# Optimization experiments

Measured on AMD Instinct MI355X. Metric: run time of the kernel, lower is better.

Reference implementation:

```python
import jax, jax.numpy as jnp
import numpy as np

NUM_HEADS = 16
EPS = 1e-6  # LinearAttention.epsilon

def setup_inputs() -> dict:
    key = jax.random.key(0)
    ks = jax.random.split(key, 10)
    B, L, D = 4, 4096, 2048
    s = 1.0 / np.sqrt(D)
    x = jax.random.normal(ks[0], (B, L, D), dtype=jnp.float32)
    attention_mask = jnp.ones((B, L), dtype=jnp.float32)
    Wq = jax.random.normal(ks[1], (D, D), dtype=jnp.float32) * s
    bq = jnp.zeros((D,), dtype=jnp.float32)
    Wk = jax.random.normal(ks[2], (D, D), dtype=jnp.float32) * s
    bk = jnp.zeros((D,), dtype=jnp.float32)
    Wv = jax.random.normal(ks[3], (D, D), dtype=jnp.float32) * s
    bv = jnp.zeros((D,), dtype=jnp.float32)
    Wo = jax.random.normal(ks[4], (D, D), dtype=jnp.float32) * s
    bo = jnp.zeros((D,), dtype=jnp.float32)
    return {"x": x, "attention_mask": attention_mask, "Wq": Wq, "bq": bq,
            "Wk": Wk, "bk": bk, "Wv": Wv, "bv": bv, "Wo": Wo, "bo": bo}

def reference(x, attention_mask, Wq, bq, Wk, bk, Wv, bv, Wo, bo):
    B, L, Dm = x.shape
    H = NUM_HEADS
    Dh = Dm // H
    # q/k/v projections -> [B, H, L, Dh]
    def proj(W, b):
        return (x @ W + b).reshape(B, L, H, Dh).transpose(0, 2, 1, 3)
    q = proj(Wq, bq)
    k = proj(Wk, bk)
    v = proj(Wv, bv)
    # feature map: elu(x) + 1
    q = jax.nn.elu(q) + 1.0
    k = jax.nn.elu(k) + 1.0
    # mask keys/values: mask [B, 1, L, 1]
    m = attention_mask[:, None, :, None]
    k = k * m
    v = v * m
    # causal linear attention via cumulative sums over sequence dim
    k_cum = jnp.cumsum(k, axis=2)          # [B,H,L,Dh]
    kv_cum = jnp.cumsum(k * v, axis=2)     # [B,H,L,Dh] (diagonal kv state, as in source)
    z = jnp.sum(q * k_cum, axis=-1) + EPS  # [B,H,L]
    z = z * attention_mask[:, None, :]
    out = (q * kv_cum) / z[..., None]      # [B,H,L,Dh]
    out = out.transpose(0, 2, 1, 3).reshape(B, L, Dm)
    return out @ Wo + bo
```

## Files before the change

kernel.cpp:

```cpp
#include <hip/hip_runtime.h>
#include <cstdint>
#include <cstddef>

#define EPS_F 1e-6f

__device__ inline unsigned short f2bf(float f) {
    union { float f; unsigned u; } v; v.f = f;
    unsigned r = v.u + 0x7fffu + ((v.u >> 16) & 1u);
    return (unsigned short)(r >> 16);
}
__device__ inline float bf2f(unsigned u16) {
    union { unsigned u; float f; } v; v.u = u16 << 16; return v.f;
}

typedef __attribute__((ext_vector_type(8))) __bf16 bf16x8;
typedef __attribute__((ext_vector_type(8))) short short8;
typedef __attribute__((ext_vector_type(4))) float floatx4;

__device__ inline void async_load16(const void* g, void* l) {
    __builtin_amdgcn_global_load_lds((const __attribute__((address_space(1))) void*)g,
                                     (__attribute__((address_space(3))) void*)l,
                                     16, 0, 0);
}

__global__ void cast_x_kernel(const float* __restrict__ in, unsigned short* __restrict__ out, int n8) {
    int i = blockIdx.x * blockDim.x + threadIdx.x;
    if (i < n8) {
        float4 a = ((const float4*)in)[2 * i];
        float4 b = ((const float4*)in)[2 * i + 1];
        short8 o;
        o[0] = (short)f2bf(a.x); o[1] = (short)f2bf(a.y);
        o[2] = (short)f2bf(a.z); o[3] = (short)f2bf(a.w);
        o[4] = (short)f2bf(b.x); o[5] = (short)f2bf(b.y);
        o[6] = (short)f2bf(b.z); o[7] = (short)f2bf(b.w);
        ((short8*)out)[i] = o;
    }
}

__global__ void transpose_cast_kernel(const float* __restrict__ W0, const float* __restrict__ W1,
                                      const float* __restrict__ W2, const float* __restrict__ W3,
                                      unsigned short* __restrict__ WtBase, int n) {
    const float* W = (blockIdx.z == 0) ? W0 : (blockIdx.z == 1) ? W1 : (blockIdx.z == 2) ? W2 : W3;
    unsigned short* Wt = WtBase + (size_t)blockIdx.z * n * n;
    __shared__ float tile[32][33];
    int bx = blockIdx.x * 32;
    int by = blockIdx.y * 32;
    int tx = threadIdx.x;
    int ty = threadIdx.y;
    #pragma unroll
    for (int i = 0; i < 32; i += 8)
        tile[ty + i][tx] = W[(size_t)(by + ty + i) * n + bx + tx];
    __syncthreads();
    #pragma unroll
    for (int i = 0; i < 32; i += 8)
        Wt[(size_t)(bx + ty + i) * n + by + tx] = f2bf(tile[tx][ty + i]);
}

#define BMT 128
#define BNT 128
#define BKT 32
#define DMODEL 2048

template<int FINAL>
__global__ __launch_bounds__(256, 2)
void gemm_kernel(const unsigned short* __restrict__ A,
                 const unsigned short* __restrict__ Bt,
                 const float* __restrict__ b0, const float* __restrict__ b1,
                 const float* __restrict__ b2,
                 const float* __restrict__ mask,
                 unsigned short* __restrict__ qo, unsigned short* __restrict__ ko,
                 unsigned short* __restrict__ vo,
                 float* __restrict__ Cf,
                 int M, int K) {
    __shared__ __align__(16) unsigned short As[BMT * BKT];
    __shared__ __align__(16) unsigned short Bs[BNT * BKT];

    const int tid  = threadIdx.x;
    const int wave = tid >> 6;
    const int lane = tid & 63;
    const int m0    = blockIdx.x * BMT;
    const int nglob = blockIdx.y * BNT;
    int mat, n0;
    const float* bias;
    unsigned short* Cb = nullptr;
    if (FINAL) {
        mat = 0; n0 = nglob; bias = b0;
    } else {
        mat  = nglob >> 11;
        n0   = nglob & (DMODEL - 1);
        bias = (mat == 0) ? b0 : (mat == 1) ? b1 : b2;
        Cb   = (mat == 0) ? qo : (mat == 1) ? ko : vo;
    }
    const int wm = (wave >> 1) * 64;
    const int wn = (wave & 1) * 64;
    const int quad  = lane >> 4;
    const int row16 = lane & 15;

    floatx4 acc[4][4] = {};

    const int sr    = wave * 32 + (lane >> 2);
    const int sslot = lane & 3;

    for (int k0 = 0; k0 < K; k0 += BKT) {
        #pragma unroll
        for (int i = 0; i < 2; i++) {
            int r = sr + i * 16;
            int c = sslot ^ (r & 3) ^ ((r >> 2) & 3);
            async_load16(A  + (size_t)(m0 + r) * K + k0 + c * 8,
                         As + (size_t)(wave * 32 + i * 16) * 32);
            async_load16(Bt + (size_t)(nglob + r) * K + k0 + c * 8,
                         Bs + (size_t)(wave * 32 + i * 16) * 32);
        }
        __syncthreads();

        bf16x8 af[4], bfr[4];
        #pragma unroll
        for (int t = 0; t < 4; t++) {
            int ra = wm + t * 16 + row16;
            int sa = quad ^ (ra & 3) ^ ((ra >> 2) & 3);
            af[t]  = __builtin_bit_cast(bf16x8, *(const short8*)(As + ra * 32 + sa * 8));
            int rb = wn + t * 16 + row16;
            int sb = quad ^ (rb & 3) ^ ((rb >> 2) & 3);
            bfr[t] = __builtin_bit_cast(bf16x8, *(const short8*)(Bs + rb * 32 + sb * 8));
        }
        #pragma unroll
        for (int i = 0; i < 4; i++)
            #pragma unroll
            for (int j = 0; j < 4; j++)
                acc[i][j] = __builtin_amdgcn_mfma_f32_16x16x32_bf16(af[i], bfr[j], acc[i][j], 0, 0, 0);
        __syncthreads();
    }

    float bcache[4];
    #pragma unroll
    for (int j = 0; j < 4; j++) bcache[j] = bias[n0 + wn + j * 16 + row16];
    #pragma unroll
    for (int i = 0; i < 4; i++) {
        #pragma unroll
        for (int r = 0; r < 4; r++) {
            int row = m0 + wm + i * 16 + quad * 4 + r;
            float mr = 1.0f;
            if (!FINAL && mat >= 1) mr = mask[row];
            #pragma unroll
            for (int j = 0; j < 4; j++) {
                int col = n0 + wn + j * 16 + row16;
                float v = acc[i][j][r] + bcache[j];
                if (FINAL) {
                    Cf[(size_t)row * DMODEL + col] = v;
                } else {
                    if (mat <= 1) v = (v > 0.f) ? (v + 1.f) : __expf(v);
                    v *= mr;
                    Cb[(size_t)row * DMODEL + col] = f2bf(v);
                }
            }
        }
    }
}

#define SL    4096
#define SD    2048
#define SH    16
#define CHUNK 64
#define NCH   64

__global__ void scan_partial_kernel(const unsigned short* __restrict__ k,
                                    const unsigned short* __restrict__ v,
                                    float* __restrict__ sumK, float* __restrict__ sumKV) {
    int blk = blockIdx.x;
    int c = blk & (NCH - 1), bh = blk >> 6;
    int b = bh >> 4, h = bh & (SH - 1);
    int lane = threadIdx.x;
    size_t base = ((size_t)(b * SL + c * CHUNK)) * SD + h * 128 + 2 * lane;
    float s0 = 0.f, s1 = 0.f, sv0 = 0.f, sv1 = 0.f;
    for (int t = 0; t < CHUNK; t++) {
        unsigned kw = *(const unsigned*)(k + base);
        unsigned vw = *(const unsigned*)(v + base);
        float k0 = bf2f(kw & 0xffff), k1 = bf2f(kw >> 16);
        float v0 = bf2f(vw & 0xffff), v1 = bf2f(vw >> 16);
        s0 += k0; s1 += k1; sv0 += k0 * v0; sv1 += k1 * v1;
        base += SD;
    }
    size_t o = ((size_t)bh * NCH + c) * 128 + 2 * lane;
    ((float2*)(sumK  + o))[0] = make_float2(s0, s1);
    ((float2*)(sumKV + o))[0] = make_float2(sv0, sv1);
}

__global__ void scan_offsets_kernel(const float* __restrict__ sumK, const float* __restrict__ sumKV,
                                    float* __restrict__ offK, float* __restrict__ offKV) {
    int bh = blockIdx.x;
    int d  = threadIdx.x;
    float aK = 0.f, aKV = 0.f;
    for (int c = 0; c < NCH; c++) {
        size_t o = ((size_t)bh * NCH + c) * 128 + d;
        float sk = sumK[o], skv = sumKV[o];
        offK[o] = aK; offKV[o] = aKV;
        aK += sk; aKV += skv;
    }
}

__global__ void scan_final_kernel(const unsigned short* __restrict__ q,
                                  const unsigned short* __restrict__ k,
                                  const unsigned short* __restrict__ v,
                                  const float* __restrict__ offK, const float* __restrict__ offKV,
                                  const float* __restrict__ mask,
                                  unsigned short* __restrict__ out) {
    int blk = blockIdx.x;
    int c = blk & (NCH - 1), bh = blk >> 6;
    int b = bh >> 4, h = bh & (SH - 1);
    int lane = threadIdx.x;
    size_t ob = ((size_t)bh * NCH + c) * 128 + 2 * lane;
    float2 kcv = ((const float2*)(offK  + ob))[0];
    float2 kvv = ((const float2*)(offKV + ob))[0];
    float kc0 = kcv.x, kc1 = kcv.y, kv0 = kvv.x, kv1 = kvv.y;
    size_t base = ((size_t)(b * SL + c * CHUNK)) * SD + h * 128 + 2 * lane;
    const float* mrow = mask + (size_t)b * SL + c * CHUNK;
    for (int t = 0; t < CHUNK; t++) {
        unsigned kw = *(const unsigned*)(k + base);
        unsigned vw = *(const unsigned*)(v + base);
        unsigned qw = *(const unsigned*)(q + base);
        float kk0 = bf2f(kw & 0xffff), kk1 = bf2f(kw >> 16);
        float vv0 = bf2f(vw & 0xffff), vv1 = bf2f(vw >> 16);
        float qq0 = bf2f(qw & 0xffff), qq1 = bf2f(qw >> 16);
        kc0 += kk0; kc1 += kk1;
        kv0 += kk0 * vv0; kv1 += kk1 * vv1;
        float p = qq0 * kc0 + qq1 * kc1;
        #pragma unroll
        for (int off = 32; off > 0; off >>= 1) p += __shfl_xor(p, off);
        float z = (p + EPS_F) * mrow[t];
        float inv = 1.0f / z;
        unsigned o0 = f2bf(qq0 * kv0 * inv);
        unsigned o1 = f2bf(qq1 * kv1 * inv);
        *(unsigned*)(out + base) = o0 | (o1 << 16);
        base += SD;
    }
}

extern "C" void kernel_launch(void* const* d_in, const int* in_sizes, int n_in,
                              void* d_out, int out_size, void* d_ws, size_t ws_size,
                              hipStream_t stream) {
    const float* x  = (const float*)d_in[0];
    const float* am = (const float*)d_in[1];
    const float* Wq = (const float*)d_in[2];
    const float* bq = (const float*)d_in[3];
    const float* Wk = (const float*)d_in[4];
    const float* bk = (const float*)d_in[5];
    const float* Wv = (const float*)d_in[6];
    const float* bv = (const float*)d_in[7];
    const float* Wo = (const float*)d_in[8];
    const float* bo = (const float*)d_in[9];
    float* out = (float*)d_out;

    const int Bb = 4, L = 4096, D = 2048;
    const int M = Bb * L;
    const size_t MD = (size_t)M * D;

    char* w = (char*)d_ws;
    unsigned short* xb    = (unsigned short*)w; w += MD * 2;
    unsigned short* qb    = (unsigned short*)w; w += MD * 2;
    unsigned short* kb    = (unsigned short*)w; w += MD * 2;
    unsigned short* vb    = (unsigned short*)w; w += MD * 2;
    unsigned short* WT    = (unsigned short*)w; w += (size_t)4 * D * D * 2;
    float* sumK  = (float*)w; w += (size_t)64 * NCH * 128 * 4;
    float* sumKV = (float*)w; w += (size_t)64 * NCH * 128 * 4;
    float* offK  = (float*)w; w += (size_t)64 * NCH * 128 * 4;
    float* offKV = (float*)w; w += (size_t)64 * NCH * 128 * 4;
    unsigned short* attnb = xb;

    int n8 = (int)(MD / 8);
    cast_x_kernel<<<(n8 + 255) / 256, 256, 0, stream>>>(x, xb, n8);
    dim3 tb(32, 8);
    dim3 tg(D / 32, D / 32, 4);
    transpose_cast_kernel<<<tg, tb, 0, stream>>>(Wq, Wk, Wv, Wo, WT, D);

    dim3 gq(M / BMT, 3 * D / BNT);
    gemm_kernel<0><<<gq, 256, 0, stream>>>(xb, WT, bq, bk, bv, am, qb, kb, vb, nullptr, M, D);

    scan_partial_kernel<<<64 * NCH, 64, 0, stream>>>(kb, vb, sumK, sumKV);
    scan_offsets_kernel<<<64, 128, 0, stream>>>(sumK, sumKV, offK, offKV);
    scan_final_kernel<<<64 * NCH, 64, 0, stream>>>(qb, kb, vb, offK, offKV, am, attnb);

    dim3 go(M / BMT, D / BNT);
    gemm_kernel<1><<<go, 256, 0, stream>>>(attnb, WT + (size_t)3 * D * D, bo, nullptr, nullptr,
                                           nullptr, nullptr, nullptr, nullptr, out, M, D);
}
```

Measured before the change: 1.033 ms.

## Double GEMM K-tile, vectorize scan partial sums, and batch scan reductions

The GEMM K tile grows from 32 to 64, with a new 8-way XOR swizzle and two MFMA sub-steps per tile, so each barrier pair covers twice the work. The scan partial kernel now does 16-byte vector loads across 4 row groups and combines them with shuffles, replacing per-row 4-byte loads. The scan final kernel unrolls 4 timesteps so loads and cross-lane reductions are batched for more ILP. The larger tiles double LDS use per block and add register pressure, which may reduce occupancy.

```diff
diff --git a/kernel.cpp b/kernel.cpp
--- a/kernel.cpp
+++ b/kernel.cpp
@@ -15,6 +15,7 @@
 
 typedef __attribute__((ext_vector_type(8))) __bf16 bf16x8;
 typedef __attribute__((ext_vector_type(8))) short short8;
+typedef __attribute__((ext_vector_type(8))) unsigned short ushort8;
 typedef __attribute__((ext_vector_type(4))) float floatx4;
 
 __device__ inline void async_load16(const void* g, void* l) {
@@ -58,7 +59,7 @@
 
 #define BMT 128
 #define BNT 128
-#define BKT 32
+#define BKT 64
 #define DMODEL 2048
 
 template<int FINAL>
@@ -98,36 +99,40 @@
 
     floatx4 acc[4][4] = {};
 
-    const int sr    = wave * 32 + (lane >> 2);
-    const int sslot = lane & 3;
+    const int srow_lo = lane >> 3;
+    const int schunk  = lane & 7;
 
     for (int k0 = 0; k0 < K; k0 += BKT) {
         #pragma unroll
-        for (int i = 0; i < 2; i++) {
-            int r = sr + i * 16;
-            int c = sslot ^ (r & 3) ^ ((r >> 2) & 3);
-            async_load16(A  + (size_t)(m0 + r) * K + k0 + c * 8,
-                         As + (size_t)(wave * 32 + i * 16) * 32);
-            async_load16(Bt + (size_t)(nglob + r) * K + k0 + c * 8,
-                         Bs + (size_t)(wave * 32 + i * 16) * 32);
+        for (int i = 0; i < 4; i++) {
+            int slot_base = wave * 256 + i * 64;
+            int r  = wave * 32 + i * 8 + srow_lo;
+            int cg = schunk ^ (r & 7);
+            const unsigned short* ga = A  + (size_t)(m0 + r) * K + k0 + cg * 8;
+            const unsigned short* gb = Bt + (size_t)(nglob + r) * K + k0 + cg * 8;
+            async_load16(ga, As + (size_t)slot_base * 8);
+            async_load16(gb, Bs + (size_t)slot_base * 8);
         }
         __syncthreads();
 
-        bf16x8 af[4], bfr[4];
-        #pragma unroll
-        for (int t = 0; t < 4; t++) {
-            int ra = wm + t * 16 + row16;
-            int sa = quad ^ (ra & 3) ^ ((ra >> 2) & 3);
-            af[t]  = __builtin_bit_cast(bf16x8, *(const short8*)(As + ra * 32 + sa * 8));
-            int rb = wn + t * 16 + row16;
-            int sb = quad ^ (rb & 3) ^ ((rb >> 2) & 3);
-            bfr[t] = __builtin_bit_cast(bf16x8, *(const short8*)(Bs + rb * 32 + sb * 8));
-        }
-        #pragma unroll
-        for (int i = 0; i < 4; i++)
+        #pragma unroll
+        for (int kk = 0; kk < 2; kk++) {
+            bf16x8 af[4], bfr[4];
             #pragma unroll
-            for (int j = 0; j < 4; j++)
-                acc[i][j] = __builtin_amdgcn_mfma_f32_16x16x32_bf16(af[i], bfr[j], acc[i][j], 0, 0, 0);
+            for (int t = 0; t < 4; t++) {
+                int ra = wm + t * 16 + row16;
+                int ca = (kk * 4 + quad) ^ (ra & 7);
+                af[t]  = __builtin_bit_cast(bf16x8, *(const short8*)(As + (size_t)ra * 64 + ca * 8));
+                int rb = wn + t * 16 + row16;
+                int cb = (kk * 4 + quad) ^ (rb & 7);
+                bfr[t] = __builtin_bit_cast(bf16x8, *(const short8*)(Bs + (size_t)rb * 64 + cb * 8));
+            }
+            #pragma unroll
+            for (int i = 0; i < 4; i++)
+                #pragma unroll
+                for (int j = 0; j < 4; j++)
+                    acc[i][j] = __builtin_amdgcn_mfma_f32_16x16x32_bf16(af[i], bfr[j], acc[i][j], 0, 0, 0);
+        }
         __syncthreads();
     }
 
@@ -170,19 +175,33 @@
     int c = blk & (NCH - 1), bh = blk >> 6;
     int b = bh >> 4, h = bh & (SH - 1);
     int lane = threadIdx.x;
-    size_t base = ((size_t)(b * SL + c * CHUNK)) * SD + h * 128 + 2 * lane;
-    float s0 = 0.f, s1 = 0.f, sv0 = 0.f, sv1 = 0.f;
-    for (int t = 0; t < CHUNK; t++) {
-        unsigned kw = *(const unsigned*)(k + base);
-        unsigned vw = *(const unsigned*)(v + base);
-        float k0 = bf2f(kw & 0xffff), k1 = bf2f(kw >> 16);
-        float v0 = bf2f(vw & 0xffff), v1 = bf2f(vw >> 16);
-        s0 += k0; s1 += k1; sv0 += k0 * v0; sv1 += k1 * v1;
-        base += SD;
-    }
-    size_t o = ((size_t)bh * NCH + c) * 128 + 2 * lane;
-    ((float2*)(sumK  + o))[0] = make_float2(s0, s1);
-    ((float2*)(sumKV + o))[0] = make_float2(sv0, sv1);
+    int tg = lane >> 4, dg = lane & 15;
+    size_t base = ((size_t)(b * SL + c * CHUNK + tg)) * SD + h * 128 + dg * 8;
+    float sk[8] = {0.f, 0.f, 0.f, 0.f, 0.f, 0.f, 0.f, 0.f};
+    float skv[8] = {0.f, 0.f, 0.f, 0.f, 0.f, 0.f, 0.f, 0.f};
+    for (int it = 0; it < CHUNK / 4; it++) {
+        ushort8 kw = *(const ushort8*)(k + base);
+        ushort8 vw = *(const ushort8*)(v + base);
+        #pragma unroll
+        for (int j = 0; j < 8; j++) {
+            float kf = bf2f(kw[j]);
+            float vf = bf2f(vw[j]);
+            sk[j] += kf; skv[j] += kf * vf;
+        }
+        base += (size_t)4 * SD;
+    }
+    #pragma unroll
+    for (int j = 0; j < 8; j++) {
+        sk[j]  += __shfl_xor(sk[j], 16);  sk[j]  += __shfl_xor(sk[j], 32);
+        skv[j] += __shfl_xor(skv[j], 16); skv[j] += __shfl_xor(skv[j], 32);
+    }
+    if (tg == 0) {
+        size_t o = ((size_t)bh * NCH + c) * 128 + dg * 8;
+        *(float4*)(sumK  + o)     = make_float4(sk[0], sk[1], sk[2], sk[3]);
+        *(float4*)(sumK  + o + 4) = make_float4(sk[4], sk[5], sk[6], sk[7]);
+        *(float4*)(sumKV + o)     = make_float4(skv[0], skv[1], skv[2], skv[3]);
+        *(float4*)(sumKV + o + 4) = make_float4(skv[4], skv[5], skv[6], skv[7]);
+    }
 }
 
 __global__ void scan_offsets_kernel(const float* __restrict__ sumK, const float* __restrict__ sumKV,
@@ -209,29 +228,45 @@
     int b = bh >> 4, h = bh & (SH - 1);
     int lane = threadIdx.x;
     size_t ob = ((size_t)bh * NCH + c) * 128 + 2 * lane;
-    float2 kcv = ((const float2*)(offK  + ob))[0];
-    float2 kvv = ((const float2*)(offKV + ob))[0];
+    float2 kcv = *(const float2*)(offK  + ob);
+    float2 kvv = *(const float2*)(offKV + ob);
     float kc0 = kcv.x, kc1 = kcv.y, kv0 = kvv.x, kv1 = kvv.y;
     size_t base = ((size_t)(b * SL + c * CHUNK)) * SD + h * 128 + 2 * lane;
     const float* mrow = mask + (size_t)b * SL + c * CHUNK;
-    for (int t = 0; t < CHUNK; t++) {
-        unsigned kw = *(const unsigned*)(k + base);
-        unsigned vw = *(const unsigned*)(v + base);
-        unsigned qw = *(const unsigned*)(q + base);
-        float kk0 = bf2f(kw & 0xffff), kk1 = bf2f(kw >> 16);
-        float vv0 = bf2f(vw & 0xffff), vv1 = bf2f(vw >> 16);
-        float qq0 = bf2f(qw & 0xffff), qq1 = bf2f(qw >> 16);
-        kc0 += kk0; kc1 += kk1;
-        kv0 += kk0 * vv0; kv1 += kk1 * vv1;
-        float p = qq0 * kc0 + qq1 * kc1;
-        #pragma unroll
-        for (int off = 32; off > 0; off >>= 1) p += __shfl_xor(p, off);
-        float z = (p + EPS_F) * mrow[t];
-        float inv = 1.0f / z;
-        unsigned o0 = f2bf(qq0 * kv0 * inv);
-        unsigned o1 = f2bf(qq1 * kv1 * inv);
-        *(unsigned*)(out + base) = o0 | (o1 << 16);
-        base += SD;
+    for (int s = 0; s < CHUNK / 4; s++) {
+        unsigned kw[4], vw[4], qw[4];
+        #pragma unroll
+        for (int u = 0; u < 4; u++) {
+            size_t a = base + (size_t)u * SD;
+            kw[u] = *(const unsigned*)(k + a);
+            vw[u] = *(const unsigned*)(v + a);
+            qw[u] = *(const unsigned*)(q + a);
+        }
+        float p[4], n0[4], n1[4];
+        #pragma unroll
+        for (int u = 0; u < 4; u++) {
+            float kk0 = bf2f(kw[u] & 0xffff), kk1 = bf2f(kw[u] >> 16);
+            float vv0 = bf2f(vw[u] & 0xffff), vv1 = bf2f(vw[u] >> 16);
+            float qq0 = bf2f(qw[u] & 0xffff), qq1 = bf2f(qw[u] >> 16);
+            kc0 += kk0; kc1 += kk1;
+            kv0 += kk0 * vv0; kv1 += kk1 * vv1;
+            p[u]  = qq0 * kc0 + qq1 * kc1;
+            n0[u] = qq0 * kv0; n1[u] = qq1 * kv1;
+        }
+        #pragma unroll
+        for (int off = 32; off > 0; off >>= 1) {
+            #pragma unroll
+            for (int u = 0; u < 4; u++) p[u] += __shfl_xor(p[u], off);
+        }
+        #pragma unroll
+        for (int u = 0; u < 4; u++) {
+            float z = (p[u] + EPS_F) * mrow[s * 4 + u];
+            float inv = 1.0f / z;
+            unsigned o0 = f2bf(n0[u] * inv);
+            unsigned o1 = f2bf(n1[u] * inv);
+            *(unsigned*)(out + base + (size_t)u * SD) = o0 | (o1 << 16);
+        }
+        base += (size_t)4 * SD;
     }
 }
 
```

After: 899.7 us. -12.9%, faster.
